# Optimization experiments

Hardware: AMD Instinct MI355X
Metric: run time of the kernel (lower is better)

## Reference

```python
import jax, jax.numpy as jnp
import numpy as np

N = 20000      # nodes
E = 640000     # edges (before self-loops)
F = 64         # base node feature len
H = 2          # heads per layer
EPS = 1e-5
NEG_SLOPE = 0.2  # PyG GATConv leaky_relu slope


def setup_inputs():
    key = jax.random.key(0)
    ks = jax.random.split(key, 16)
    s = 0.1
    x = jax.random.normal(ks[0], (N, F), jnp.float32)
    edge_index = jax.random.randint(ks[1], (2, E), 0, N, dtype=jnp.int64)
    # layer 1: in=F, heads=H, out-per-head C1=F -> out dim H*F=128
    C1 = F
    W1 = jax.random.normal(ks[2], (F, H * C1), jnp.float32) * s
    att_src1 = jax.random.normal(ks[3], (H, C1), jnp.float32) * s
    att_dst1 = jax.random.normal(ks[4], (H, C1), jnp.float32) * s
    bias1 = jnp.zeros((H * C1,), jnp.float32)
    gamma1 = jnp.ones((H * C1,), jnp.float32)
    beta1 = jnp.zeros((H * C1,), jnp.float32)
    # layer 2: in=H*F=128, heads=H, out-per-head C2=H*F -> out dim H*H*F=256
    C2 = H * F
    W2 = jax.random.normal(ks[5], (H * C1, H * C2), jnp.float32) * s
    att_src2 = jax.random.normal(ks[6], (H, C2), jnp.float32) * s
    att_dst2 = jax.random.normal(ks[7], (H, C2), jnp.float32) * s
    bias2 = jnp.zeros((H * C2,), jnp.float32)
    gamma2 = jnp.ones((H * C2,), jnp.float32)
    beta2 = jnp.zeros((H * C2,), jnp.float32)
    return {"x": x, "edge_index": edge_index,
            "W1": W1, "att_src1": att_src1, "att_dst1": att_dst1, "bias1": bias1,
            "gamma1": gamma1, "beta1": beta1,
            "W2": W2, "att_src2": att_src2, "att_dst2": att_dst2, "bias2": bias2,
            "gamma2": gamma2, "beta2": beta2}


def _gat_conv(x, src, dst, W, att_src, att_dst, bias):
    # PyG GATConv (concat=True, add_self_loops already applied to src/dst)
    n = x.shape[0]
    h, c = att_src.shape
    hx = (x @ W).reshape(n, h, c)                       # [N,H,C]
    a_s = jnp.einsum('nhc,hc->nh', hx, att_src)         # [N,H]
    a_d = jnp.einsum('nhc,hc->nh', hx, att_dst)
    e = a_s[src] + a_d[dst]                             # [E',H]
    e = jnp.where(e > 0, e, NEG_SLOPE * e)              # leaky relu
    # segment softmax over incoming edges of each target node
    m = jax.ops.segment_max(e, dst, num_segments=n)     # [N,H]
    p = jnp.exp(e - m[dst])
    z = jax.ops.segment_sum(p, dst, num_segments=n)     # [N,H]
    alpha = p / z[dst]                                  # [E',H]
    msg = hx[src] * alpha[:, :, None]                   # [E',H,C]
    out = jax.ops.segment_sum(msg, dst, num_segments=n) # [N,H,C]
    return out.reshape(n, h * c) + bias


def _batch_norm(x, gamma, beta):
    mu = x.mean(axis=0)
    var = x.var(axis=0)  # biased, matches torch BN normalization
    return (x - mu) * jax.lax.rsqrt(var + EPS) * gamma + beta


def reference(x, edge_index, W1, att_src1, att_dst1, bias1, gamma1, beta1,
              W2, att_src2, att_dst2, bias2, gamma2, beta2):
    loops = jnp.arange(N, dtype=edge_index.dtype)
    src = jnp.concatenate([edge_index[0], loops])
    dst = jnp.concatenate([edge_index[1], loops])
    h = _gat_conv(x, src, dst, W1, att_src1, att_dst1, bias1)
    h = jax.nn.relu(_batch_norm(h, gamma1, beta1))
    h = _gat_conv(h, src, dst, W2, att_src2, att_dst2, bias2)
    h = jax.nn.relu(_batch_norm(h, gamma2, beta2))
    return h
```

## Files before the change

### kernel.cpp

```cpp
#include <hip/hip_runtime.h>
#include <hip/hip_bf16.h>
#include <math.h>

#define NN 20000
#define ER 640000
#define ET 660000
#define HH 2
#define D1 128
#define D2 256
#define EPSV 1e-5f
#define SLOPE 0.2f

typedef __attribute__((ext_vector_type(8))) short bf16x8;
typedef __attribute__((ext_vector_type(4))) float f32x4;


__device__ __forceinline__ int detect64(const void* ei) {
  const int* p = (const int*)ei;
  return (p[1] | p[3] | p[5] | p[7]) == 0;
}
__device__ __forceinline__ int clampn(int v) { return v < 0 ? 0 : (v >= NN ? NN-1 : v); }
__device__ __forceinline__ float bf16_lo(unsigned int u){ return __uint_as_float(u<<16); }
__device__ __forceinline__ float bf16_hi(unsigned int u){ return __uint_as_float(u & 0xffff0000u); }

__global__ void k_front(const void* ei, const float* W1, const float* W2,
                        __hip_bfloat16* W1t, __hip_bfloat16* W2c, int* dpart, int* gcount) {
  extern __shared__ int hist[];
  int b = blockIdx.x, t = threadIdx.x;
  if (b == 0 && t == 0) *gcount = 0;
  if (b < 160) {
    int i = b*256 + t;
    if (i < 8192) {
      int n = i >> 6, k = i & 63;
      W1t[i] = __float2bfloat16(W1[k*128 + n]);
    } else {
      int i2 = i - 8192;
      int kc = i2 >> 13, n = (i2 >> 5) & 255, kk = i2 & 31;
      W2c[i2] = __float2bfloat16(W2[(kc*32 + kk)*256 + n]);
    }
    return;
  }
  int db = b - 160;
  for (int i = t; i < NN; i += 256) hist[i] = 0;
  __syncthreads();
  int is64 = detect64(ei);
  int base = db * 80000;
  if (is64) {
    const long long* p64 = (const long long*)ei;
    for (int i = base + t*4; i < base + 80000; i += 1024) {
      uint4 qa = *(const uint4*)(p64 + ER + i);
      uint4 qb = *(const uint4*)(p64 + ER + i + 2);
      atomicAdd(&hist[clampn((int)qa.x)], 1);
      atomicAdd(&hist[clampn((int)qa.z)], 1);
      atomicAdd(&hist[clampn((int)qb.x)], 1);
      atomicAdd(&hist[clampn((int)qb.z)], 1);
    }
  } else {
    const int* p32 = (const int*)ei;
    for (int i = base + t*4; i < base + 80000; i += 1024) {
      uint4 q = *(const uint4*)(p32 + ER + i);
      atomicAdd(&hist[clampn((int)q.x)], 1);
      atomicAdd(&hist[clampn((int)q.y)], 1);
      atomicAdd(&hist[clampn((int)q.z)], 1);
      atomicAdd(&hist[clampn((int)q.w)], 1);
    }
  }
  __syncthreads();
  for (int i = t; i < NN; i += 256) dpart[db*NN + i] = hist[i];
}

__global__ __launch_bounds__(256) void k_alloc(const int* dpart, int* begv, int* endv,
                                               int* cursor, int* gcount, float* bnz) {
  __shared__ int wsum[4], wbase[4];
  int gid = blockIdx.x*256 + threadIdx.x;
  if (gid < 768) bnz[gid] = 0.f;
  int d = 0;
  if (gid < NN) {
    d = 1;
    #pragma unroll
    for (int bb = 0; bb < 8; bb++) d += dpart[bb*NN + gid];
  }
  int lane = threadIdx.x & 63, w = threadIdx.x >> 6;
  int v = d;
  #pragma unroll
  for (int o = 1; o < 64; o <<= 1) {
    int u = __shfl_up(v, o);
    if (lane >= o) v += u;
  }
  if (lane == 63) wsum[w] = v;
  __syncthreads();
  if (threadIdx.x == 0) {
    int s0 = wsum[0], s1 = wsum[1], s2 = wsum[2], s3 = wsum[3];
    int b = atomicAdd(gcount, s0 + s1 + s2 + s3);
    wbase[0] = b; wbase[1] = b + s0; wbase[2] = b + s0 + s1; wbase[3] = b + s0 + s1 + s2;
  }
  __syncthreads();
  if (gid < NN) {
    int beg = wbase[w] + v - d;
    begv[gid] = beg; cursor[gid] = beg; endv[gid] = beg + d;
  }
}

__global__ void k_scatter(const void* ei, int* cursor, int* srcs) {
  int i0 = (blockIdx.x*256 + threadIdx.x)*4;
  if (i0 >= ET) return;
  int s[4], d[4];
  if (i0 >= ER) {
    #pragma unroll
    for (int k = 0; k < 4; k++) { s[k] = i0 + k - ER; d[k] = s[k]; }
  } else if (detect64(ei)) {
    const long long* p64 = (const long long*)ei;
    uint4 qa = *(const uint4*)(p64 + i0);
    uint4 qb = *(const uint4*)(p64 + i0 + 2);
    uint4 ra = *(const uint4*)(p64 + ER + i0);
    uint4 rb = *(const uint4*)(p64 + ER + i0 + 2);
    s[0]=clampn((int)qa.x); s[1]=clampn((int)qa.z); s[2]=clampn((int)qb.x); s[3]=clampn((int)qb.z);
    d[0]=clampn((int)ra.x); d[1]=clampn((int)ra.z); d[2]=clampn((int)rb.x); d[3]=clampn((int)rb.z);
  } else {
    const int* p32 = (const int*)ei;
    uint4 qs = *(const uint4*)(p32 + i0);
    uint4 qd = *(const uint4*)(p32 + ER + i0);
    s[0]=clampn((int)qs.x); s[1]=clampn((int)qs.y); s[2]=clampn((int)qs.z); s[3]=clampn((int)qs.w);
    d[0]=clampn((int)qd.x); d[1]=clampn((int)qd.y); d[2]=clampn((int)qd.z); d[3]=clampn((int)qd.w);
  }
  #pragma unroll
  for (int k = 0; k < 4; k++) {
    int pos = atomicAdd(&cursor[d[k]], 1);
    srcs[pos] = s[k];
  }
}

__global__ __launch_bounds__(256) void k_gemm1f(const float* x, const __hip_bfloat16* W1t,
                                                const float* att_s1, const float* att_d1,
                                                __hip_bfloat16* hxb, float2* as1, float2* ad1) {
  __shared__ __hip_bfloat16 As[64][72];
  __shared__ __hip_bfloat16 Bs[128][72];
  __shared__ float asred[4][64], adred[4][64];
  int t = threadIdx.x;
  int m0 = blockIdx.x * 64;
  for (int i = t; i < 512; i += 256) {
    int r = i >> 3, s = i & 7;
    int gr = m0 + r; if (gr >= NN) gr = NN - 1;
    float4 f0 = ((const float4*)(x + (size_t)gr*64))[s*2];
    float4 f1 = ((const float4*)(x + (size_t)gr*64))[s*2+1];
    __hip_bfloat16 hb[8] = {
      __float2bfloat16(f0.x), __float2bfloat16(f0.y), __float2bfloat16(f0.z), __float2bfloat16(f0.w),
      __float2bfloat16(f1.x), __float2bfloat16(f1.y), __float2bfloat16(f1.z), __float2bfloat16(f1.w)};
    *(uint4*)&As[r][s*8] = *(uint4*)hb;
  }
  for (int i = t; i < 1024; i += 256) {
    int r = i >> 3, s = i & 7;
    *(uint4*)&Bs[r][s*8] = ((const uint4*)(W1t + (size_t)r*64))[s];
  }
  __syncthreads();
  int w = t >> 6, lane = t & 63;
  int lm = lane & 15, q = lane >> 4;
  f32x4 acc[4][2];
  #pragma unroll
  for (int rt = 0; rt < 4; rt++)
    #pragma unroll
    for (int ct = 0; ct < 2; ct++) acc[rt][ct] = (f32x4){0.f,0.f,0.f,0.f};
  #pragma unroll
  for (int kc = 0; kc < 2; kc++) {
    bf16x8 bfr[2];
    #pragma unroll
    for (int ct = 0; ct < 2; ct++)
      bfr[ct] = *(const bf16x8*)&Bs[w*32 + ct*16 + lm][kc*32 + q*8];
    #pragma unroll
    for (int rt = 0; rt < 4; rt++) {
      bf16x8 a = *(const bf16x8*)&As[rt*16 + lm][kc*32 + q*8];
      acc[rt][0] = __builtin_amdgcn_mfma_f32_16x16x32_bf16(a, bfr[0], acc[rt][0], 0, 0, 0);
      acc[rt][1] = __builtin_amdgcn_mfma_f32_16x16x32_bf16(a, bfr[1], acc[rt][1], 0, 0, 0);
    }
  }
  #pragma unroll
  for (int rt = 0; rt < 4; rt++)
    #pragma unroll
    for (int ct = 0; ct < 2; ct++)
      #pragma unroll
      for (int rg = 0; rg < 4; rg++) {
        int row = m0 + rt*16 + q*4 + rg;
        int col = w*32 + ct*16 + lm;
        if (row < NN) hxb[(size_t)row*128 + col] = __float2bfloat16(acc[rt][ct][rg]);
      }
  float asc[2], adc[2];
  #pragma unroll
  for (int ct = 0; ct < 2; ct++) {
    int col = w*32 + ct*16 + lm;
    asc[ct] = att_s1[col]; adc[ct] = att_d1[col];
  }
  #pragma unroll
  for (int rt = 0; rt < 4; rt++)
    #pragma unroll
    for (int rg = 0; rg < 4; rg++) {
      float ps = acc[rt][0][rg]*asc[0] + acc[rt][1][rg]*asc[1];
      float pd = acc[rt][0][rg]*adc[0] + acc[rt][1][rg]*adc[1];
      #pragma unroll
      for (int o = 1; o < 16; o <<= 1) { ps += __shfl_xor(ps, o); pd += __shfl_xor(pd, o); }
      if (lm == 0) { int row = rt*16 + q*4 + rg; asred[w][row] = ps; adred[w][row] = pd; }
    }
  __syncthreads();
  if (t < 64) {
    int row = m0 + t;
    if (row < NN) {
      as1[row] = make_float2(asred[0][t] + asred[1][t], asred[2][t] + asred[3][t]);
      ad1[row] = make_float2(adred[0][t] + adred[1][t], adred[2][t] + adred[3][t]);
    }
  }
}

__global__ __launch_bounds__(256) void k_gemm2f(const float* out1, const __hip_bfloat16* W2c,
                                                const float* bns1, const float* bnq1,
                                                const float* gamma1, const float* beta1,
                                                const float* att_s2, const float* att_d2,
                                                __hip_bfloat16* hxb, float2* as2, float2* ad2) {
  __shared__ __hip_bfloat16 As[64][136];
  __shared__ __hip_bfloat16 Bs[256][40];
  __shared__ float AB[2][128];
  __shared__ float asred[4][64], adred[4][64];
  int t = threadIdx.x;
  int m0 = blockIdx.x * 64;
  if (t < 128) {
    float mean = bns1[t]*(1.f/NN);
    float var  = bnq1[t]*(1.f/NN) - mean*mean;
    float A = rsqrtf(var + EPSV)*gamma1[t];
    AB[0][t] = A; AB[1][t] = beta1[t] - mean*A;
  }
  __syncthreads();
  for (int i = t; i < 1024; i += 256) {
    int r = i >> 4, s = i & 15;
    int gr = m0 + r; if (gr >= NN) gr = NN - 1;
    float4 f0 = ((const float4*)(out1 + (size_t)gr*128))[s*2];
    float4 f1 = ((const float4*)(out1 + (size_t)gr*128))[s*2+1];
    int c = s*8;
    float v[8] = {f0.x,f0.y,f0.z,f0.w,f1.x,f1.y,f1.z,f1.w};
    __hip_bfloat16 hb[8];
    #pragma unroll
    for (int k = 0; k < 8; k++)
      hb[k] = __float2bfloat16(fmaxf(v[k]*AB[0][c+k] + AB[1][c+k], 0.f));
    *(uint4*)&As[r][s*8] = *(uint4*)hb;
  }
  int w = t >> 6, lane = t & 63;
  int lm = lane & 15, q = lane >> 4;
  f32x4 acc[4][4];
  #pragma unroll
  for (int rt = 0; rt < 4; rt++)
    #pragma unroll
    for (int ct = 0; ct < 4; ct++) acc[rt][ct] = (f32x4){0.f,0.f,0.f,0.f};
  for (int kc = 0; kc < 4; kc++) {
    __syncthreads();
    for (int i = t; i < 1024; i += 256) {
      int r = i >> 2, s = i & 3;
      *(uint4*)&Bs[r][s*8] = ((const uint4*)(W2c + ((size_t)kc*256 + r)*32))[s];
    }
    __syncthreads();
    bf16x8 bfr[4];
    #pragma unroll
    for (int ct = 0; ct < 4; ct++)
      bfr[ct] = *(const bf16x8*)&Bs[w*64 + ct*16 + lm][q*8];
    #pragma unroll
    for (int rt = 0; rt < 4; rt++) {
      bf16x8 a = *(const bf16x8*)&As[rt*16 + lm][kc*32 + q*8];
      #pragma unroll
      for (int ct = 0; ct < 4; ct++)
        acc[rt][ct] = __builtin_amdgcn_mfma_f32_16x16x32_bf16(a, bfr[ct], acc[rt][ct], 0, 0, 0);
    }
  }
  #pragma unroll
  for (int rt = 0; rt < 4; rt++)
    #pragma unroll
    for (int ct = 0; ct < 4; ct++)
      #pragma unroll
      for (int rg = 0; rg < 4; rg++) {
        int row = m0 + rt*16 + q*4 + rg;
        int col = w*64 + ct*16 + lm;
        if (row < NN) hxb[(size_t)row*256 + col] = __float2bfloat16(acc[rt][ct][rg]);
      }
  float asc[4], adc[4];
  #pragma unroll
  for (int ct = 0; ct < 4; ct++) {
    int col = w*64 + ct*16 + lm;
    asc[ct] = att_s2[col]; adc[ct] = att_d2[col];
  }
  #pragma unroll
  for (int rt = 0; rt < 4; rt++)
    #pragma unroll
    for (int rg = 0; rg < 4; rg++) {
      float ps = acc[rt][0][rg]*asc[0] + acc[rt][1][rg]*asc[1]
               + acc[rt][2][rg]*asc[2] + acc[rt][3][rg]*asc[3];
      float pd = acc[rt][0][rg]*adc[0] + acc[rt][1][rg]*adc[1]
               + acc[rt][2][rg]*adc[2] + acc[rt][3][rg]*adc[3];
      #pragma unroll
      for (int o = 1; o < 16; o <<= 1) { ps += __shfl_xor(ps, o); pd += __shfl_xor(pd, o); }
      if (lm == 0) { int row = rt*16 + q*4 + rg; asred[w][row] = ps; adred[w][row] = pd; }
    }
  __syncthreads();
  if (t < 64) {
    int row = m0 + t;
    if (row < NN) {
      as2[row] = make_float2(asred[0][t] + asred[1][t], asred[2][t] + asred[3][t]);
      ad2[row] = make_float2(adred[0][t] + adred[1][t], adred[2][t] + adred[3][t]);
    }
  }
}

__global__ __launch_bounds__(64) void k_agg1(const int* begv, const int* endv, const int* srcs,
                                             const float2* asv, const float2* adv,
                                             const uint2* hx, const float* bias, float* out) {
  __shared__ float2 sp[2][64];
  int n = blockIdx.x, t = threadIdx.x;
  int l = t & 31, eo = t >> 5;
  int h = l >> 4;
  float2 ad = adv[n];
  int beg = begv[n], end = endv[n];
  float a0=0.f,a1=0.f,a2=0.f,a3=0.f,z0=0.f,z1=0.f;
  for (int cb = beg; cb < end; cb += 64) {
    int len = end - cb; if (len > 64) len = 64;
    if (t < len) {
      int s = srcs[cb + t];
      float2 as = asv[s];
      float e0 = as.x + ad.x, e1 = as.y + ad.y;
      e0 = e0 > 0.f ? e0 : SLOPE*e0;
      e1 = e1 > 0.f ? e1 : SLOPE*e1;
      float p0 = __expf(e0), p1 = __expf(e1);
      sp[0][t] = make_float2(__int_as_float(s), p0);
      sp[1][t] = make_float2(__int_as_float(s), p1);
      z0 += p0; z1 += p1;
    }
    __syncthreads();
    for (int j = eo; j < len; j += 2) {
      float2 v = sp[h][j];
      uint2 u = hx[(size_t)__float_as_int(v.x)*32 + l];
      a0 += v.y*bf16_lo(u.x); a1 += v.y*bf16_hi(u.x);
      a2 += v.y*bf16_lo(u.y); a3 += v.y*bf16_hi(u.y);
    }
    __syncthreads();
  }
  a0 += __shfl_down(a0, 32); a1 += __shfl_down(a1, 32);
  a2 += __shfl_down(a2, 32); a3 += __shfl_down(a3, 32);
  #pragma unroll
  for (int o = 1; o < 64; o <<= 1) { z0 += __shfl_xor(z0, o); z1 += __shfl_xor(z1, o); }
  if (t < 32) {
    float inv = 1.f / (h ? z1 : z0);
    float4 b4 = ((const float4*)bias)[t];
    float4 o4 = { a0*inv + b4.x, a1*inv + b4.y, a2*inv + b4.z, a3*inv + b4.w };
    ((float4*)(out + (size_t)n*D1))[t] = o4;
  }
}

__global__ __launch_bounds__(64) void k_agg2(const int* begv, const int* endv, const int* srcs,
                                             const float2* asv, const float2* adv,
                                             const uint2* hx, const float* bias, float* out) {
  __shared__ float2 sp[2][64];
  int n = blockIdx.x, t = threadIdx.x;
  int h = t >> 5;
  float2 ad = adv[n];
  int beg = begv[n], end = endv[n];
  float a0=0.f,a1=0.f,a2=0.f,a3=0.f,z0=0.f,z1=0.f;
  for (int cb = beg; cb < end; cb += 64) {
    int len = end - cb; if (len > 64) len = 64;
    if (t < len) {
      int s = srcs[cb + t];
      float2 as = asv[s];
      float e0 = as.x + ad.x, e1 = as.y + ad.y;
      e0 = e0 > 0.f ? e0 : SLOPE*e0;
      e1 = e1 > 0.f ? e1 : SLOPE*e1;
      float p0 = __expf(e0), p1 = __expf(e1);
      sp[0][t] = make_float2(__int_as_float(s), p0);
      sp[1][t] = make_float2(__int_as_float(s), p1);
      z0 += p0; z1 += p1;
    }
    __syncthreads();
    int j = 0;
    for (; j + 1 < len; j += 2) {
      float2 v0 = sp[h][j], v1 = sp[h][j+1];
      uint2 u0 = hx[(size_t)__float_as_int(v0.x)*64 + t];
      uint2 u1 = hx[(size_t)__float_as_int(v1.x)*64 + t];
      a0 += v0.y*bf16_lo(u0.x) + v1.y*bf16_lo(u1.x);
      a1 += v0.y*bf16_hi(u0.x) + v1.y*bf16_hi(u1.x);
      a2 += v0.y*bf16_lo(u0.y) + v1.y*bf16_lo(u1.y);
      a3 += v0.y*bf16_hi(u0.y) + v1.y*bf16_hi(u1.y);
    }
    for (; j < len; j++) {
      float2 v = sp[h][j];
      uint2 u = hx[(size_t)__float_as_int(v.x)*64 + t];
      a0 += v.y*bf16_lo(u.x); a1 += v.y*bf16_hi(u.x);
      a2 += v.y*bf16_lo(u.y); a3 += v.y*bf16_hi(u.y);
    }
    __syncthreads();
  }
  #pragma unroll
  for (int o = 1; o < 64; o <<= 1) { z0 += __shfl_xor(z0, o); z1 += __shfl_xor(z1, o); }
  float inv = 1.f / (h ? z1 : z0);
  float4 b4 = ((const float4*)bias)[t];
  float4 o4 = { a0*inv + b4.x, a1*inv + b4.y, a2*inv + b4.z, a3*inv + b4.w };
  ((float4*)(out + (size_t)n*D2))[t] = o4;
}

template<int D>
__global__ void k_bnstats(const float* x, float* bnsum, float* bnsq) {
  const int ROWS = 100;
  int c = threadIdx.x;
  int r0 = blockIdx.x * ROWS;
  float s = 0.f, s2 = 0.f;
  for (int r = 0; r < ROWS; r++) {
    float v = x[(size_t)(r0 + r)*D + c];
    s += v; s2 += v*v;
  }
  atomicAdd(&bnsum[c], s);
  atomicAdd(&bnsq[c], s2);
}

__global__ void k_bnapply2(const float* x, const float* bnsum, const float* bnsq,
                           const float* gamma, const float* beta, float* out) {
  int i = blockIdx.x*blockDim.x + threadIdx.x;
  if (i >= NN*D2/4) return;
  int c = (i & 63) * 4;
  float4 v = ((const float4*)x)[i];
  float r[4] = {v.x, v.y, v.z, v.w};
  #pragma unroll
  for (int k = 0; k < 4; k++) {
    float mean = bnsum[c+k] * (1.f/NN);
    float var  = bnsq[c+k] * (1.f/NN) - mean*mean;
    float o = (r[k] - mean) * rsqrtf(var + EPSV) * gamma[c+k] + beta[c+k];
    r[k] = o > 0.f ? o : 0.f;
  }
  float4 o4 = {r[0], r[1], r[2], r[3]};
  ((float4*)out)[i] = o4;
}

extern "C" void kernel_launch(void* const* d_in, const int* in_sizes, int n_in,
                              void* d_out, int out_size, void* d_ws, size_t ws_size,
                              hipStream_t stream) {
  const float* x      = (const float*)d_in[0];
  const void*  ei     = d_in[1];
  const float* W1     = (const float*)d_in[2];
  const float* att_s1 = (const float*)d_in[3];
  const float* att_d1 = (const float*)d_in[4];
  const float* bias1  = (const float*)d_in[5];
  const float* gamma1 = (const float*)d_in[6];
  const float* beta1  = (const float*)d_in[7];
  const float* W2     = (const float*)d_in[8];
  const float* att_s2 = (const float*)d_in[9];
  const float* att_d2 = (const float*)d_in[10];
  const float* bias2  = (const float*)d_in[11];
  const float* gamma2 = (const float*)d_in[12];
  const float* beta2  = (const float*)d_in[13];

  char* p = (char*)d_ws;
  __hip_bfloat16* hx1b = (__hip_bfloat16*)p; p += (size_t)NN*D1*2;
  __hip_bfloat16* hx2b = (__hip_bfloat16*)p; p += (size_t)NN*D2*2;
  __hip_bfloat16* W1t  = (__hip_bfloat16*)p; p += 8192*2;
  __hip_bfloat16* W2c  = (__hip_bfloat16*)p; p += 32768*2;
  float* out1 = (float*)p; p += (size_t)NN*D1*4;
  float* out2 = (float*)p; p += (size_t)NN*D2*4;
  float2* as1 = (float2*)p; p += (size_t)NN*8;
  float2* ad1 = (float2*)p; p += (size_t)NN*8;
  float2* as2 = (float2*)p; p += (size_t)NN*8;
  float2* ad2 = (float2*)p; p += (size_t)NN*8;
  float* bns1 = (float*)p; p += D1*4;
  float* bnq1 = (float*)p; p += D1*4;
  float* bns2 = (float*)p; p += D2*4;
  float* bnq2 = (float*)p; p += D2*4;
  int* dpart  = (int*)p; p += (size_t)8*NN*4;
  int* begv   = (int*)p; p += NN*4;
  int* endv   = (int*)p; p += NN*4;
  int* cursor = (int*)p; p += NN*4;
  int* gcount = (int*)p; p += 16*4;
  int* srcs   = (int*)p; p += (size_t)ET*4;

  k_front<<<168, 256, NN*sizeof(int), stream>>>(ei, W1, W2, W1t, W2c, dpart, gcount);
  k_alloc<<<(NN+255)/256, 256, 0, stream>>>(dpart, begv, endv, cursor, gcount, bns1);
  k_scatter<<<(ET/4 + 255)/256, 256, 0, stream>>>(ei, cursor, srcs);

  k_gemm1f<<<(NN+63)/64, 256, 0, stream>>>(x, W1t, att_s1, att_d1, hx1b, as1, ad1);
  k_agg1<<<NN, 64, 0, stream>>>(begv, endv, srcs, as1, ad1, (const uint2*)hx1b, bias1, out1);
  k_bnstats<D1><<<200, D1, 0, stream>>>(out1, bns1, bnq1);

  k_gemm2f<<<(NN+63)/64, 256, 0, stream>>>(out1, W2c, bns1, bnq1, gamma1, beta1,
                                           att_s2, att_d2, hx2b, as2, ad2);
  k_agg2<<<NN, 64, 0, stream>>>(begv, endv, srcs, as2, ad2, (const uint2*)hx2b, bias2, out2);
  k_bnstats<D2><<<200, D2, 0, stream>>>(out2, bns2, bnq2);
  k_bnapply2<<<(NN*D2/4 + 255)/256, 256, 0, stream>>>(out2, bns2, bnq2, gamma2, beta2,
                                                      (float*)d_out);
}
```

Baseline: 274.6 us.

## Fuse whole GAT pipeline into one persistent cooperative kernel with grid syncs

Replaces the chain of about ten separate kernel launches with a single persistent cooperative kernel that walks seven phases, separated by grid-wide syncs. The edge histogram now uses packed 16-bit counters in 64 chunks. BatchNorm statistics are accumulated inside the aggregation phases instead of in separate stats kernels. Weight bf16 conversion is folded into each GEMM tile, and aggregation now processes one node per wave across a grid-stride loop. This removes launch gaps and extra passes over the output, at the cost of lower occupancy, grid-sync overhead, and redundant weight conversion in every tile.

```diff
diff --git a/kernel.cpp b/kernel.cpp
--- a/kernel.cpp
+++ b/kernel.cpp
@@ -1,19 +1,40 @@
 #include <hip/hip_runtime.h>
 #include <hip/hip_bf16.h>
+#include <hip/hip_cooperative_groups.h>
 #include <math.h>
 
 #define NN 20000
 #define ER 640000
 #define ET 660000
-#define HH 2
 #define D1 128
 #define D2 256
 #define EPSV 1e-5f
 #define SLOPE 0.2f
+#define NT1 313
+#define NHIST 64
+#define HCH 10000
 
 typedef __attribute__((ext_vector_type(8))) short bf16x8;
 typedef __attribute__((ext_vector_type(4))) float f32x4;
 
+namespace cg = cooperative_groups;
+
+struct P {
+  const float* x; const void* ei;
+  const float* W1; const float* att_s1; const float* att_d1; const float* bias1;
+  const float* gamma1; const float* beta1;
+  const float* W2; const float* att_s2; const float* att_d2; const float* bias2;
+  const float* gamma2; const float* beta2;
+  __hip_bfloat16* hx1b; __hip_bfloat16* hx2b;
+  float* out1; float* out2;
+  float2* as1; float2* ad1; float2* as2; float2* ad2;
+  float* bn;
+  unsigned int* dpart;
+  int* begv; int* endv; int* cursor; int* gcount;
+  int* srcs;
+  float* dout;
+  int ph_lo, ph_hi, coop;
+};
 
 __device__ __forceinline__ int detect64(const void* ei) {
   const int* p = (const int*)ei;
@@ -23,138 +44,29 @@
 __device__ __forceinline__ float bf16_lo(unsigned int u){ return __uint_as_float(u<<16); }
 __device__ __forceinline__ float bf16_hi(unsigned int u){ return __uint_as_float(u & 0xffff0000u); }
 
-__global__ void k_front(const void* ei, const float* W1, const float* W2,
-                        __hip_bfloat16* W1t, __hip_bfloat16* W2c, int* dpart, int* gcount) {
-  extern __shared__ int hist[];
-  int b = blockIdx.x, t = threadIdx.x;
-  if (b == 0 && t == 0) *gcount = 0;
-  if (b < 160) {
-    int i = b*256 + t;
-    if (i < 8192) {
-      int n = i >> 6, k = i & 63;
-      W1t[i] = __float2bfloat16(W1[k*128 + n]);
-    } else {
-      int i2 = i - 8192;
-      int kc = i2 >> 13, n = (i2 >> 5) & 255, kk = i2 & 31;
-      W2c[i2] = __float2bfloat16(W2[(kc*32 + kk)*256 + n]);
-    }
-    return;
-  }
-  int db = b - 160;
-  for (int i = t; i < NN; i += 256) hist[i] = 0;
-  __syncthreads();
-  int is64 = detect64(ei);
-  int base = db * 80000;
-  if (is64) {
-    const long long* p64 = (const long long*)ei;
-    for (int i = base + t*4; i < base + 80000; i += 1024) {
-      uint4 qa = *(const uint4*)(p64 + ER + i);
-      uint4 qb = *(const uint4*)(p64 + ER + i + 2);
-      atomicAdd(&hist[clampn((int)qa.x)], 1);
-      atomicAdd(&hist[clampn((int)qa.z)], 1);
-      atomicAdd(&hist[clampn((int)qb.x)], 1);
-      atomicAdd(&hist[clampn((int)qb.z)], 1);
-    }
-  } else {
-    const int* p32 = (const int*)ei;
-    for (int i = base + t*4; i < base + 80000; i += 1024) {
-      uint4 q = *(const uint4*)(p32 + ER + i);
-      atomicAdd(&hist[clampn((int)q.x)], 1);
-      atomicAdd(&hist[clampn((int)q.y)], 1);
-      atomicAdd(&hist[clampn((int)q.z)], 1);
-      atomicAdd(&hist[clampn((int)q.w)], 1);
-    }
-  }
-  __syncthreads();
-  for (int i = t; i < NN; i += 256) dpart[db*NN + i] = hist[i];
-}
-
-__global__ __launch_bounds__(256) void k_alloc(const int* dpart, int* begv, int* endv,
-                                               int* cursor, int* gcount, float* bnz) {
-  __shared__ int wsum[4], wbase[4];
-  int gid = blockIdx.x*256 + threadIdx.x;
-  if (gid < 768) bnz[gid] = 0.f;
-  int d = 0;
-  if (gid < NN) {
-    d = 1;
-    #pragma unroll
-    for (int bb = 0; bb < 8; bb++) d += dpart[bb*NN + gid];
-  }
-  int lane = threadIdx.x & 63, w = threadIdx.x >> 6;
-  int v = d;
-  #pragma unroll
-  for (int o = 1; o < 64; o <<= 1) {
-    int u = __shfl_up(v, o);
-    if (lane >= o) v += u;
-  }
-  if (lane == 63) wsum[w] = v;
-  __syncthreads();
-  if (threadIdx.x == 0) {
-    int s0 = wsum[0], s1 = wsum[1], s2 = wsum[2], s3 = wsum[3];
-    int b = atomicAdd(gcount, s0 + s1 + s2 + s3);
-    wbase[0] = b; wbase[1] = b + s0; wbase[2] = b + s0 + s1; wbase[3] = b + s0 + s1 + s2;
-  }
-  __syncthreads();
-  if (gid < NN) {
-    int beg = wbase[w] + v - d;
-    begv[gid] = beg; cursor[gid] = beg; endv[gid] = beg + d;
-  }
-}
-
-__global__ void k_scatter(const void* ei, int* cursor, int* srcs) {
-  int i0 = (blockIdx.x*256 + threadIdx.x)*4;
-  if (i0 >= ET) return;
-  int s[4], d[4];
-  if (i0 >= ER) {
-    #pragma unroll
-    for (int k = 0; k < 4; k++) { s[k] = i0 + k - ER; d[k] = s[k]; }
-  } else if (detect64(ei)) {
-    const long long* p64 = (const long long*)ei;
-    uint4 qa = *(const uint4*)(p64 + i0);
-    uint4 qb = *(const uint4*)(p64 + i0 + 2);
-    uint4 ra = *(const uint4*)(p64 + ER + i0);
-    uint4 rb = *(const uint4*)(p64 + ER + i0 + 2);
-    s[0]=clampn((int)qa.x); s[1]=clampn((int)qa.z); s[2]=clampn((int)qb.x); s[3]=clampn((int)qb.z);
-    d[0]=clampn((int)ra.x); d[1]=clampn((int)ra.z); d[2]=clampn((int)rb.x); d[3]=clampn((int)rb.z);
-  } else {
-    const int* p32 = (const int*)ei;
-    uint4 qs = *(const uint4*)(p32 + i0);
-    uint4 qd = *(const uint4*)(p32 + ER + i0);
-    s[0]=clampn((int)qs.x); s[1]=clampn((int)qs.y); s[2]=clampn((int)qs.z); s[3]=clampn((int)qs.w);
-    d[0]=clampn((int)qd.x); d[1]=clampn((int)qd.y); d[2]=clampn((int)qd.z); d[3]=clampn((int)qd.w);
-  }
-  #pragma unroll
-  for (int k = 0; k < 4; k++) {
-    int pos = atomicAdd(&cursor[d[k]], 1);
-    srcs[pos] = s[k];
-  }
-}
-
-__global__ __launch_bounds__(256) void k_gemm1f(const float* x, const __hip_bfloat16* W1t,
-                                                const float* att_s1, const float* att_d1,
-                                                __hip_bfloat16* hxb, float2* as1, float2* ad1) {
-  __shared__ __hip_bfloat16 As[64][72];
-  __shared__ __hip_bfloat16 Bs[128][72];
-  __shared__ float asred[4][64], adred[4][64];
+__device__ void gemm1_tile(int u, const P& p, char* smem) {
+  auto As = (__hip_bfloat16 (*)[72])smem;
+  auto Bs = (__hip_bfloat16 (*)[72])(smem + 9216);
+  float* asred = (float*)(smem + 27648);
+  float* adred = (float*)(smem + 28672);
   int t = threadIdx.x;
-  int m0 = blockIdx.x * 64;
+  int m0 = u * 64;
   for (int i = t; i < 512; i += 256) {
     int r = i >> 3, s = i & 7;
     int gr = m0 + r; if (gr >= NN) gr = NN - 1;
-    float4 f0 = ((const float4*)(x + (size_t)gr*64))[s*2];
-    float4 f1 = ((const float4*)(x + (size_t)gr*64))[s*2+1];
+    float4 f0 = ((const float4*)(p.x + (size_t)gr*64))[s*2];
+    float4 f1 = ((const float4*)(p.x + (size_t)gr*64))[s*2+1];
     __hip_bfloat16 hb[8] = {
       __float2bfloat16(f0.x), __float2bfloat16(f0.y), __float2bfloat16(f0.z), __float2bfloat16(f0.w),
       __float2bfloat16(f1.x), __float2bfloat16(f1.y), __float2bfloat16(f1.z), __float2bfloat16(f1.w)};
     *(uint4*)&As[r][s*8] = *(uint4*)hb;
   }
-  for (int i = t; i < 1024; i += 256) {
-    int r = i >> 3, s = i & 7;
-    *(uint4*)&Bs[r][s*8] = ((const uint4*)(W1t + (size_t)r*64))[s];
-  }
-  __syncthreads();
-  int w = t >> 6, lane = t & 63;
-  int lm = lane & 15, q = lane >> 4;
+  for (int i = t; i < 8192; i += 256) {
+    int n = i & 127, k = i >> 7;
+    Bs[n][k] = __float2bfloat16(p.W1[k*128 + n]);
+  }
+  __syncthreads();
+  int w = t >> 6, lane = t & 63, lm = lane & 15, q = lane >> 4;
   f32x4 acc[4][2];
   #pragma unroll
   for (int rt = 0; rt < 4; rt++)
@@ -181,13 +93,13 @@
       for (int rg = 0; rg < 4; rg++) {
         int row = m0 + rt*16 + q*4 + rg;
         int col = w*32 + ct*16 + lm;
-        if (row < NN) hxb[(size_t)row*128 + col] = __float2bfloat16(acc[rt][ct][rg]);
+        if (row < NN) p.hx1b[(size_t)row*128 + col] = __float2bfloat16(acc[rt][ct][rg]);
       }
   float asc[2], adc[2];
   #pragma unroll
   for (int ct = 0; ct < 2; ct++) {
     int col = w*32 + ct*16 + lm;
-    asc[ct] = att_s1[col]; adc[ct] = att_d1[col];
+    asc[ct] = p.att_s1[col]; adc[ct] = p.att_d1[col];
   }
   #pragma unroll
   for (int rt = 0; rt < 4; rt++)
@@ -197,51 +109,182 @@
       float pd = acc[rt][0][rg]*adc[0] + acc[rt][1][rg]*adc[1];
       #pragma unroll
       for (int o = 1; o < 16; o <<= 1) { ps += __shfl_xor(ps, o); pd += __shfl_xor(pd, o); }
-      if (lm == 0) { int row = rt*16 + q*4 + rg; asred[w][row] = ps; adred[w][row] = pd; }
+      if (lm == 0) { int row = rt*16 + q*4 + rg; asred[w*64+row] = ps; adred[w*64+row] = pd; }
     }
   __syncthreads();
   if (t < 64) {
     int row = m0 + t;
     if (row < NN) {
-      as1[row] = make_float2(asred[0][t] + asred[1][t], asred[2][t] + asred[3][t]);
-      ad1[row] = make_float2(adred[0][t] + adred[1][t], adred[2][t] + adred[3][t]);
-    }
-  }
-}
-
-__global__ __launch_bounds__(256) void k_gemm2f(const float* out1, const __hip_bfloat16* W2c,
-                                                const float* bns1, const float* bnq1,
-                                                const float* gamma1, const float* beta1,
-                                                const float* att_s2, const float* att_d2,
-                                                __hip_bfloat16* hxb, float2* as2, float2* ad2) {
-  __shared__ __hip_bfloat16 As[64][136];
-  __shared__ __hip_bfloat16 Bs[256][40];
-  __shared__ float AB[2][128];
-  __shared__ float asred[4][64], adred[4][64];
+      p.as1[row] = make_float2(asred[t] + asred[64+t], asred[128+t] + asred[192+t]);
+      p.ad1[row] = make_float2(adred[t] + adred[64+t], adred[128+t] + adred[192+t]);
+    }
+  }
+  __syncthreads();
+}
+
+__device__ void hist_unit(int db, const P& p, char* smem) {
+  unsigned int* hist = (unsigned int*)smem;
   int t = threadIdx.x;
-  int m0 = blockIdx.x * 64;
+  for (int i = t; i < HCH; i += 256) hist[i] = 0;
+  __syncthreads();
+  int base = db * HCH;
+  if (detect64(p.ei)) {
+    const long long* q = (const long long*)p.ei + ER;
+    for (int i = base + t; i < base + HCH; i += 256) {
+      int d = clampn((int)q[i]);
+      atomicAdd(&hist[d>>1], 1u << ((d&1)*16));
+    }
+  } else {
+    const int* q = (const int*)p.ei + ER;
+    for (int i = base + t; i < base + HCH; i += 256) {
+      int d = clampn(q[i]);
+      atomicAdd(&hist[d>>1], 1u << ((d&1)*16));
+    }
+  }
+  __syncthreads();
+  for (int i = t; i < HCH; i += 256) p.dpart[db*HCH + i] = hist[i];
+  __syncthreads();
+}
+
+__device__ void alloc_unit(int u, const P& p, char* smem) {
+  int* wsum  = (int*)smem;
+  int* wbase = wsum + 4;
+  int t = threadIdx.x;
+  int gid = u*256 + t;
+  int d = 0;
+  if (gid < NN) {
+    d = 1;
+    int half = (gid & 1) * 16;
+    int idx = gid >> 1;
+    for (int db = 0; db < NHIST; db++)
+      d += (p.dpart[db*HCH + idx] >> half) & 0xffff;
+  }
+  int lane = t & 63, w = t >> 6;
+  int v = d;
+  #pragma unroll
+  for (int o = 1; o < 64; o <<= 1) {
+    int uu = __shfl_up(v, o);
+    if (lane >= o) v += uu;
+  }
+  if (lane == 63) wsum[w] = v;
+  __syncthreads();
+  if (t == 0) {
+    int s0 = wsum[0], s1 = wsum[1], s2 = wsum[2], s3 = wsum[3];
+    int b = atomicAdd(p.gcount, s0 + s1 + s2 + s3);
+    wbase[0] = b; wbase[1] = b + s0; wbase[2] = b + s0 + s1; wbase[3] = b + s0 + s1 + s2;
+  }
+  __syncthreads();
+  if (gid < NN) {
+    int beg = wbase[w] + v - d;
+    p.begv[gid] = beg; p.cursor[gid] = beg; p.endv[gid] = beg + d;
+  }
+  __syncthreads();
+}
+
+__device__ void scatter_phase(const P& p, int gtid, int GT) {
+  int is64 = detect64(p.ei);
+  for (int u = gtid; u < ET/4; u += GT) {
+    int i0 = u*4;
+    int s[4], d[4];
+    if (i0 >= ER) {
+      #pragma unroll
+      for (int k = 0; k < 4; k++) { s[k] = i0 + k - ER; d[k] = s[k]; }
+    } else if (is64) {
+      const long long* p64 = (const long long*)p.ei;
+      uint4 qa = *(const uint4*)(p64 + i0);
+      uint4 qb = *(const uint4*)(p64 + i0 + 2);
+      uint4 ra = *(const uint4*)(p64 + ER + i0);
+      uint4 rb = *(const uint4*)(p64 + ER + i0 + 2);
+      s[0]=clampn((int)qa.x); s[1]=clampn((int)qa.z); s[2]=clampn((int)qb.x); s[3]=clampn((int)qb.z);
+      d[0]=clampn((int)ra.x); d[1]=clampn((int)ra.z); d[2]=clampn((int)rb.x); d[3]=clampn((int)rb.z);
+    } else {
+      const int* p32 = (const int*)p.ei;
+      uint4 qs = *(const uint4*)(p32 + i0);
+      uint4 qd = *(const uint4*)(p32 + ER + i0);
+      s[0]=clampn((int)qs.x); s[1]=clampn((int)qs.y); s[2]=clampn((int)qs.z); s[3]=clampn((int)qs.w);
+      d[0]=clampn((int)qd.x); d[1]=clampn((int)qd.y); d[2]=clampn((int)qd.z); d[3]=clampn((int)qd.w);
+    }
+    #pragma unroll
+    for (int k = 0; k < 4; k++) {
+      int pos = atomicAdd(&p.cursor[d[k]], 1);
+      p.srcs[pos] = s[k];
+    }
+  }
+}
+
+__device__ void agg1_phase(const P& p, char* smem, int B) {
+  float* bnacc = (float*)smem;
+  int t = threadIdx.x;
+  for (int i = t; i < 256; i += 256) bnacc[i] = 0.f;
+  __syncthreads();
+  int wid = t >> 6, lane = t & 63, h = lane >> 5;
+  const unsigned int* hx = (const unsigned int*)p.hx1b;
+  for (int n = blockIdx.x*4 + wid; n < NN; n += B*4) {
+    float2 ad = p.ad1[n];
+    int beg = p.begv[n], end = p.endv[n];
+    float a0=0.f, a1=0.f, z0=0.f, z1=0.f;
+    for (int cb = beg; cb < end; cb += 64) {
+      int len = end - cb; if (len > 64) len = 64;
+      int st = 0; float p0 = 0.f, p1 = 0.f;
+      if (lane < len) {
+        st = p.srcs[cb + lane];
+        float2 as = p.as1[st];
+        float e0 = as.x + ad.x, e1 = as.y + ad.y;
+        e0 = e0 > 0.f ? e0 : SLOPE*e0;
+        e1 = e1 > 0.f ? e1 : SLOPE*e1;
+        p0 = __expf(e0); p1 = __expf(e1);
+        z0 += p0; z1 += p1;
+      }
+      for (int j = 0; j < len; j++) {
+        int sj = __shfl(st, j);
+        float q0 = __shfl(p0, j), q1 = __shfl(p1, j);
+        float pj = h ? q1 : q0;
+        unsigned int uu = hx[(size_t)sj*64 + lane];
+        a0 += pj*bf16_lo(uu); a1 += pj*bf16_hi(uu);
+      }
+    }
+    #pragma unroll
+    for (int o = 1; o < 64; o <<= 1) { z0 += __shfl_xor(z0, o); z1 += __shfl_xor(z1, o); }
+    float inv = 1.f / (h ? z1 : z0);
+    float v0 = a0*inv + p.bias1[2*lane];
+    float v1 = a1*inv + p.bias1[2*lane+1];
+    ((float2*)(p.out1 + (size_t)n*D1))[lane] = make_float2(v0, v1);
+    atomicAdd(&bnacc[2*lane], v0);       atomicAdd(&bnacc[2*lane+1], v1);
+    atomicAdd(&bnacc[128+2*lane], v0*v0); atomicAdd(&bnacc[128+2*lane+1], v1*v1);
+  }
+  __syncthreads();
+  for (int i = t; i < 256; i += 256) atomicAdd(&p.bn[i], bnacc[i]);
+}
+
+__device__ void gemm2_tile(int u, const P& p, char* smem) {
+  auto As = (__hip_bfloat16 (*)[136])smem;
+  auto Bs = (__hip_bfloat16 (*)[40])(smem + 17408);
+  float* AB    = (float*)(smem + 37888);
+  float* asred = (float*)(smem + 38912);
+  float* adred = (float*)(smem + 39936);
+  int t = threadIdx.x;
+  int m0 = u * 64;
   if (t < 128) {
-    float mean = bns1[t]*(1.f/NN);
-    float var  = bnq1[t]*(1.f/NN) - mean*mean;
-    float A = rsqrtf(var + EPSV)*gamma1[t];
-    AB[0][t] = A; AB[1][t] = beta1[t] - mean*A;
+    float mean = p.bn[t]*(1.f/NN);
+    float var  = p.bn[128+t]*(1.f/NN) - mean*mean;
+    float A = rsqrtf(var + EPSV)*p.gamma1[t];
+    AB[t] = A; AB[128+t] = p.beta1[t] - mean*A;
   }
   __syncthreads();
   for (int i = t; i < 1024; i += 256) {
     int r = i >> 4, s = i & 15;
     int gr = m0 + r; if (gr >= NN) gr = NN - 1;
-    float4 f0 = ((const float4*)(out1 + (size_t)gr*128))[s*2];
-    float4 f1 = ((const float4*)(out1 + (size_t)gr*128))[s*2+1];
+    float4 f0 = ((const float4*)(p.out1 + (size_t)gr*128))[s*2];
+    float4 f1 = ((const float4*)(p.out1 + (size_t)gr*128))[s*2+1];
     int c = s*8;
     float v[8] = {f0.x,f0.y,f0.z,f0.w,f1.x,f1.y,f1.z,f1.w};
     __hip_bfloat16 hb[8];
     #pragma unroll
     for (int k = 0; k < 8; k++)
-      hb[k] = __float2bfloat16(fmaxf(v[k]*AB[0][c+k] + AB[1][c+k], 0.f));
+      hb[k] = __float2bfloat16(fmaxf(v[k]*AB[c+k] + AB[128+c+k], 0.f));
     *(uint4*)&As[r][s*8] = *(uint4*)hb;
   }
-  int w = t >> 6, lane = t & 63;
-  int lm = lane & 15, q = lane >> 4;
+  int w = t >> 6, lane = t & 63, lm = lane & 15, q = lane >> 4;
   f32x4 acc[4][4];
   #pragma unroll
   for (int rt = 0; rt < 4; rt++)
@@ -249,9 +292,9 @@
     for (int ct = 0; ct < 4; ct++) acc[rt][ct] = (f32x4){0.f,0.f,0.f,0.f};
   for (int kc = 0; kc < 4; kc++) {
     __syncthreads();
-    for (int i = t; i < 1024; i += 256) {
-      int r = i >> 2, s = i & 3;
-      *(uint4*)&Bs[r][s*8] = ((const uint4*)(W2c + ((size_t)kc*256 + r)*32))[s];
+    for (int i = t; i < 8192; i += 256) {
+      int n = i & 255, kk = i >> 8;
+      Bs[n][kk] = __float2bfloat16(p.W2[(kc*32 + kk)*256 + n]);
     }
     __syncthreads();
     bf16x8 bfr[4];
@@ -274,13 +317,13 @@
       for (int rg = 0; rg < 4; rg++) {
         int row = m0 + rt*16 + q*4 + rg;
         int col = w*64 + ct*16 + lm;
-        if (row < NN) hxb[(size_t)row*256 + col] = __float2bfloat16(acc[rt][ct][rg]);
+        if (row < NN) p.hx2b[(size_t)row*256 + col] = __float2bfloat16(acc[rt][ct][rg]);
       }
   float asc[4], adc[4];
   #pragma unroll
   for (int ct = 0; ct < 4; ct++) {
     int col = w*64 + ct*16 + lm;
-    asc[ct] = att_s2[col]; adc[ct] = att_d2[col];
+    asc[ct] = p.att_s2[col]; adc[ct] = p.att_d2[col];
   }
   #pragma unroll
   for (int rt = 0; rt < 4; rt++)
@@ -292,195 +335,171 @@
                + acc[rt][2][rg]*adc[2] + acc[rt][3][rg]*adc[3];
       #pragma unroll
       for (int o = 1; o < 16; o <<= 1) { ps += __shfl_xor(ps, o); pd += __shfl_xor(pd, o); }
-      if (lm == 0) { int row = rt*16 + q*4 + rg; asred[w][row] = ps; adred[w][row] = pd; }
+      if (lm == 0) { int row = rt*16 + q*4 + rg; asred[w*64+row] = ps; adred[w*64+row] = pd; }
     }
   __syncthreads();
   if (t < 64) {
     int row = m0 + t;
     if (row < NN) {
-      as2[row] = make_float2(asred[0][t] + asred[1][t], asred[2][t] + asred[3][t]);
-      ad2[row] = make_float2(adred[0][t] + adred[1][t], adred[2][t] + adred[3][t]);
-    }
-  }
-}
-
-__global__ __launch_bounds__(64) void k_agg1(const int* begv, const int* endv, const int* srcs,
-                                             const float2* asv, const float2* adv,
-                                             const uint2* hx, const float* bias, float* out) {
-  __shared__ float2 sp[2][64];
-  int n = blockIdx.x, t = threadIdx.x;
-  int l = t & 31, eo = t >> 5;
-  int h = l >> 4;
-  float2 ad = adv[n];
-  int beg = begv[n], end = endv[n];
-  float a0=0.f,a1=0.f,a2=0.f,a3=0.f,z0=0.f,z1=0.f;
-  for (int cb = beg; cb < end; cb += 64) {
-    int len = end - cb; if (len > 64) len = 64;
-    if (t < len) {
-      int s = srcs[cb + t];
-      float2 as = asv[s];
-      float e0 = as.x + ad.x, e1 = as.y + ad.y;
-      e0 = e0 > 0.f ? e0 : SLOPE*e0;
-      e1 = e1 > 0.f ? e1 : SLOPE*e1;
-      float p0 = __expf(e0), p1 = __expf(e1);
-      sp[0][t] = make_float2(__int_as_float(s), p0);
-      sp[1][t] = make_float2(__int_as_float(s), p1);
-      z0 += p0; z1 += p1;
-    }
-    __syncthreads();
-    for (int j = eo; j < len; j += 2) {
-      float2 v = sp[h][j];
-      uint2 u = hx[(size_t)__float_as_int(v.x)*32 + l];
-      a0 += v.y*bf16_lo(u.x); a1 += v.y*bf16_hi(u.x);
-      a2 += v.y*bf16_lo(u.y); a3 += v.y*bf16_hi(u.y);
-    }
-    __syncthreads();
-  }
-  a0 += __shfl_down(a0, 32); a1 += __shfl_down(a1, 32);
-  a2 += __shfl_down(a2, 32); a3 += __shfl_down(a3, 32);
-  #pragma unroll
-  for (int o = 1; o < 64; o <<= 1) { z0 += __shfl_xor(z0, o); z1 += __shfl_xor(z1, o); }
-  if (t < 32) {
+      p.as2[row] = make_float2(asred[t] + asred[64+t], asred[128+t] + asred[192+t]);
+      p.ad2[row] = make_float2(adred[t] + adred[64+t], adred[128+t] + adred[192+t]);
+    }
+  }
+  __syncthreads();
+}
+
+__device__ void agg2_phase(const P& p, char* smem, int B) {
+  float* bnacc = (float*)smem;
+  int t = threadIdx.x;
+  for (int i = t; i < 512; i += 256) bnacc[i] = 0.f;
+  __syncthreads();
+  int wid = t >> 6, lane = t & 63, h = lane >> 5;
+  const uint2* hx = (const uint2*)p.hx2b;
+  for (int n = blockIdx.x*4 + wid; n < NN; n += B*4) {
+    float2 ad = p.ad2[n];
+    int beg = p.begv[n], end = p.endv[n];
+    float a0=0.f,a1=0.f,a2=0.f,a3=0.f,z0=0.f,z1=0.f;
+    for (int cb = beg; cb < end; cb += 64) {
+      int len = end - cb; if (len > 64) len = 64;
+      int st = 0; float p0 = 0.f, p1 = 0.f;
+      if (lane < len) {
+        st = p.srcs[cb + lane];
+        float2 as = p.as2[st];
+        float e0 = as.x + ad.x, e1 = as.y + ad.y;
+        e0 = e0 > 0.f ? e0 : SLOPE*e0;
+        e1 = e1 > 0.f ? e1 : SLOPE*e1;
+        p0 = __expf(e0); p1 = __expf(e1);
+        z0 += p0; z1 += p1;
+      }
+      for (int j = 0; j < len; j++) {
+        int sj = __shfl(st, j);
+        float q0 = __shfl(p0, j), q1 = __shfl(p1, j);
+        float pj = h ? q1 : q0;
+        uint2 uu = hx[(size_t)sj*64 + lane];
+        a0 += pj*bf16_lo(uu.x); a1 += pj*bf16_hi(uu.x);
+        a2 += pj*bf16_lo(uu.y); a3 += pj*bf16_hi(uu.y);
+      }
+    }
+    #pragma unroll
+    for (int o = 1; o < 64; o <<= 1) { z0 += __shfl_xor(z0, o); z1 += __shfl_xor(z1, o); }
     float inv = 1.f / (h ? z1 : z0);
-    float4 b4 = ((const float4*)bias)[t];
+    float4 b4 = ((const float4*)p.bias2)[lane];
     float4 o4 = { a0*inv + b4.x, a1*inv + b4.y, a2*inv + b4.z, a3*inv + b4.w };
-    ((float4*)(out + (size_t)n*D1))[t] = o4;
-  }
-}
-
-__global__ __launch_bounds__(64) void k_agg2(const int* begv, const int* endv, const int* srcs,
-                                             const float2* asv, const float2* adv,
-                                             const uint2* hx, const float* bias, float* out) {
-  __shared__ float2 sp[2][64];
-  int n = blockIdx.x, t = threadIdx.x;
-  int h = t >> 5;
-  float2 ad = adv[n];
-  int beg = begv[n], end = endv[n];
-  float a0=0.f,a1=0.f,a2=0.f,a3=0.f,z0=0.f,z1=0.f;
-  for (int cb = beg; cb < end; cb += 64) {
-    int len = end - cb; if (len > 64) len = 64;
-    if (t < len) {
-      int s = srcs[cb + t];
-      float2 as = asv[s];
-      float e0 = as.x + ad.x, e1 = as.y + ad.y;
-      e0 = e0 > 0.f ? e0 : SLOPE*e0;
-      e1 = e1 > 0.f ? e1 : SLOPE*e1;
-      float p0 = __expf(e0), p1 = __expf(e1);
-      sp[0][t] = make_float2(__int_as_float(s), p0);
-      sp[1][t] = make_float2(__int_as_float(s), p1);
-      z0 += p0; z1 += p1;
-    }
-    __syncthreads();
-    int j = 0;
-    for (; j + 1 < len; j += 2) {
-      float2 v0 = sp[h][j], v1 = sp[h][j+1];
-      uint2 u0 = hx[(size_t)__float_as_int(v0.x)*64 + t];
-      uint2 u1 = hx[(size_t)__float_as_int(v1.x)*64 + t];
-      a0 += v0.y*bf16_lo(u0.x) + v1.y*bf16_lo(u1.x);
-      a1 += v0.y*bf16_hi(u0.x) + v1.y*bf16_hi(u1.x);
-      a2 += v0.y*bf16_lo(u0.y) + v1.y*bf16_lo(u1.y);
-      a3 += v0.y*bf16_hi(u0.y) + v1.y*bf16_hi(u1.y);
-    }
-    for (; j < len; j++) {
-      float2 v = sp[h][j];
-      uint2 u = hx[(size_t)__float_as_int(v.x)*64 + t];
-      a0 += v.y*bf16_lo(u.x); a1 += v.y*bf16_hi(u.x);
-      a2 += v.y*bf16_lo(u.y); a3 += v.y*bf16_hi(u.y);
-    }
-    __syncthreads();
-  }
-  #pragma unroll
-  for (int o = 1; o < 64; o <<= 1) { z0 += __shfl_xor(z0, o); z1 += __shfl_xor(z1, o); }
-  float inv = 1.f / (h ? z1 : z0);
-  float4 b4 = ((const float4*)bias)[t];
-  float4 o4 = { a0*inv + b4.x, a1*inv + b4.y, a2*inv + b4.z, a3*inv + b4.w };
-  ((float4*)(out + (size_t)n*D2))[t] = o4;
-}
-
-template<int D>
-__global__ void k_bnstats(const float* x, float* bnsum, float* bnsq) {
-  const int ROWS = 100;
-  int c = threadIdx.x;
-  int r0 = blockIdx.x * ROWS;
-  float s = 0.f, s2 = 0.f;
-  for (int r = 0; r < ROWS; r++) {
-    float v = x[(size_t)(r0 + r)*D + c];
-    s += v; s2 += v*v;
-  }
-  atomicAdd(&bnsum[c], s);
-  atomicAdd(&bnsq[c], s2);
-}
-
-__global__ void k_bnapply2(const float* x, const float* bnsum, const float* bnsq,
-                           const float* gamma, const float* beta, float* out) {
-  int i = blockIdx.x*blockDim.x + threadIdx.x;
-  if (i >= NN*D2/4) return;
-  int c = (i & 63) * 4;
-  float4 v = ((const float4*)x)[i];
-  float r[4] = {v.x, v.y, v.z, v.w};
-  #pragma unroll
-  for (int k = 0; k < 4; k++) {
-    float mean = bnsum[c+k] * (1.f/NN);
-    float var  = bnsq[c+k] * (1.f/NN) - mean*mean;
-    float o = (r[k] - mean) * rsqrtf(var + EPSV) * gamma[c+k] + beta[c+k];
-    r[k] = o > 0.f ? o : 0.f;
-  }
-  float4 o4 = {r[0], r[1], r[2], r[3]};
-  ((float4*)out)[i] = o4;
+    ((float4*)(p.out2 + (size_t)n*D2))[lane] = o4;
+    int c = 4*lane;
+    atomicAdd(&bnacc[c],   o4.x); atomicAdd(&bnacc[c+1], o4.y);
+    atomicAdd(&bnacc[c+2], o4.z); atomicAdd(&bnacc[c+3], o4.w);
+    atomicAdd(&bnacc[256+c],   o4.x*o4.x); atomicAdd(&bnacc[256+c+1], o4.y*o4.y);
+    atomicAdd(&bnacc[256+c+2], o4.z*o4.z); atomicAdd(&bnacc[256+c+3], o4.w*o4.w);
+  }
+  __syncthreads();
+  for (int i = t; i < 512; i += 256) atomicAdd(&p.bn[256+i], bnacc[i]);
+}
+
+__global__ __launch_bounds__(256, 4) void k_mono(P p) {
+  __shared__ __attribute__((aligned(16))) char smem[40960];
+  cg::grid_group g = cg::this_grid();
+  int B = gridDim.x, bid = blockIdx.x, t = threadIdx.x;
+  int gtid = bid*256 + t, GT = B*256;
+  for (int ph = p.ph_lo; ph < p.ph_hi; ph++) {
+    switch (ph) {
+      case 0:
+        for (int u = bid; u < NT1 + NHIST + 1; u += B) {
+          if (u < NT1) gemm1_tile(u, p, smem);
+          else if (u < NT1 + NHIST) hist_unit(u - NT1, p, smem);
+          else {
+            if (t == 0) *p.gcount = 0;
+            for (int i = t; i < 768; i += 256) p.bn[i] = 0.f;
+          }
+        }
+        break;
+      case 1:
+        for (int u = bid; u < (NN + 255)/256; u += B) alloc_unit(u, p, smem);
+        break;
+      case 2: scatter_phase(p, gtid, GT); break;
+      case 3: agg1_phase(p, smem, B); break;
+      case 4:
+        for (int u = bid; u < NT1; u += B) gemm2_tile(u, p, smem);
+        break;
+      case 5: agg2_phase(p, smem, B); break;
+      case 6:
+        for (int i = gtid; i < NN*64; i += GT) {
+          int c = (i & 63)*4;
+          float4 v = ((const float4*)p.out2)[i];
+          float r[4] = {v.x, v.y, v.z, v.w};
+          #pragma unroll
+          for (int k = 0; k < 4; k++) {
+            float mean = p.bn[256+c+k]*(1.f/NN);
+            float var  = p.bn[512+c+k]*(1.f/NN) - mean*mean;
+            float o = (r[k] - mean)*rsqrtf(var + EPSV)*p.gamma2[c+k] + p.beta2[c+k];
+            r[k] = o > 0.f ? o : 0.f;
+          }
+          float4 o4 = {r[0], r[1], r[2], r[3]};
+          ((float4*)p.dout)[i] = o4;
+        }
+        break;
+    }
+    if (p.coop && ph + 1 < p.ph_hi) g.sync();
+  }
 }
 
 extern "C" void kernel_launch(void* const* d_in, const int* in_sizes, int n_in,
                               void* d_out, int out_size, void* d_ws, size_t ws_size,
                               hipStream_t stream) {
-  const float* x      = (const float*)d_in[0];
-  const void*  ei     = d_in[1];
-  const float* W1     = (const float*)d_in[2];
-  const float* att_s1 = (const float*)d_in[3];
-  const float* att_d1 = (const float*)d_in[4];
-  const float* bias1  = (const float*)d_in[5];
-  const float* gamma1 = (const float*)d_in[6];
-  const float* beta1  = (const float*)d_in[7];
-  const float* W2     = (const float*)d_in[8];
-  const float* att_s2 = (const float*)d_in[9];
-  const float* att_d2 = (const float*)d_in[10];
-  const float* bias2  = (const float*)d_in[11];
-  const float* gamma2 = (const float*)d_in[12];
-  const float* beta2  = (const float*)d_in[13];
+  P prm;
+  prm.x      = (const float*)d_in[0];
+  prm.ei     = d_in[1];
+  prm.W1     = (const float*)d_in[2];
+  prm.att_s1 = (const float*)d_in[3];
+  prm.att_d1 = (const float*)d_in[4];
+  prm.bias1  = (const float*)d_in[5];
+  prm.gamma1 = (const float*)d_in[6];
+  prm.beta1  = (const float*)d_in[7];
+  prm.W2     = (const float*)d_in[8];
+  prm.att_s2 = (const float*)d_in[9];
+  prm.att_d2 = (const float*)d_in[10];
+  prm.bias2  = (const float*)d_in[11];
+  prm.gamma2 = (const float*)d_in[12];
+  prm.beta2  = (const float*)d_in[13];
 
   char* p = (char*)d_ws;
-  __hip_bfloat16* hx1b = (__hip_bfloat16*)p; p += (size_t)NN*D1*2;
-  __hip_bfloat16* hx2b = (__hip_bfloat16*)p; p += (size_t)NN*D2*2;
-  __hip_bfloat16* W1t  = (__hip_bfloat16*)p; p += 8192*2;
-  __hip_bfloat16* W2c  = (__hip_bfloat16*)p; p += 32768*2;
-  float* out1 = (float*)p; p += (size_t)NN*D1*4;
-  float* out2 = (float*)p; p += (size_t)NN*D2*4;
-  float2* as1 = (float2*)p; p += (size_t)NN*8;
-  float2* ad1 = (float2*)p; p += (size_t)NN*8;
-  float2* as2 = (float2*)p; p += (size_t)NN*8;
-  float2* ad2 = (float2*)p; p += (size_t)NN*8;
-  float* bns1 = (float*)p; p += D1*4;
-  float* bnq1 = (float*)p; p += D1*4;
-  float* bns2 = (float*)p; p += D2*4;
-  float* bnq2 = (float*)p; p += D2*4;
-  int* dpart  = (int*)p; p += (size_t)8*NN*4;
-  int* begv   = (int*)p; p += NN*4;
-  int* endv   = (int*)p; p += NN*4;
-  int* cursor = (int*)p; p += NN*4;
-  int* gcount = (int*)p; p += 16*4;
-  int* srcs   = (int*)p; p += (size_t)ET*4;
-
-  k_front<<<168, 256, NN*sizeof(int), stream>>>(ei, W1, W2, W1t, W2c, dpart, gcount);
-  k_alloc<<<(NN+255)/256, 256, 0, stream>>>(dpart, begv, endv, cursor, gcount, bns1);
-  k_scatter<<<(ET/4 + 255)/256, 256, 0, stream>>>(ei, cursor, srcs);
-
-  k_gemm1f<<<(NN+63)/64, 256, 0, stream>>>(x, W1t, att_s1, att_d1, hx1b, as1, ad1);
-  k_agg1<<<NN, 64, 0, stream>>>(begv, endv, srcs, as1, ad1, (const uint2*)hx1b, bias1, out1);
-  k_bnstats<D1><<<200, D1, 0, stream>>>(out1, bns1, bnq1);
-
-  k_gemm2f<<<(NN+63)/64, 256, 0, stream>>>(out1, W2c, bns1, bnq1, gamma1, beta1,
-                                           att_s2, att_d2, hx2b, as2, ad2);
-  k_agg2<<<NN, 64, 0, stream>>>(begv, endv, srcs, as2, ad2, (const uint2*)hx2b, bias2, out2);
-  k_bnstats<D2><<<200, D2, 0, stream>>>(out2, bns2, bnq2);
-  k_bnapply2<<<(NN*D2/4 + 255)/256, 256, 0, stream>>>(out2, bns2, bnq2, gamma2, beta2,
-                                                      (float*)d_out);
-}
+  prm.hx1b = (__hip_bfloat16*)p; p += (size_t)NN*D1*2;
+  prm.hx2b = (__hip_bfloat16*)p; p += (size_t)NN*D2*2;
+  prm.out1 = (float*)p; p += (size_t)NN*D1*4;
+  prm.out2 = (float*)p; p += (size_t)NN*D2*4;
+  prm.as1  = (float2*)p; p += (size_t)NN*8;
+  prm.ad1  = (float2*)p; p += (size_t)NN*8;
+  prm.as2  = (float2*)p; p += (size_t)NN*8;
+  prm.ad2  = (float2*)p; p += (size_t)NN*8;
+  prm.bn   = (float*)p; p += 768*4;
+  prm.dpart = (unsigned int*)p; p += (size_t)NHIST*HCH*4;
+  prm.begv   = (int*)p; p += NN*4;
+  prm.endv   = (int*)p; p += NN*4;
+  prm.cursor = (int*)p; p += NN*4;
+  prm.gcount = (int*)p; p += 16*4;
+  prm.srcs   = (int*)p; p += (size_t)ET*4;
+  prm.dout = (float*)d_out;
+
+  int dev = 0; hipGetDevice(&dev);
+  int ncu = 0;
+  hipDeviceGetAttribute(&ncu, hipDeviceAttributeMultiprocessorCount, dev);
+  if (ncu <= 0) ncu = 256;
+  int coopSup = 0;
+  hipDeviceGetAttribute(&coopSup, hipDeviceAttributeCooperativeLaunch, dev);
+  int nb = 0;
+  if (hipOccupancyMaxActiveBlocksPerMultiprocessor(&nb, k_mono, 256, 0) != hipSuccess || nb < 1)
+    nb = 1;
+  if (nb > 4) nb = 4;
+  int grid = nb * ncu;
+
+  if (coopSup) {
+    prm.ph_lo = 0; prm.ph_hi = 7; prm.coop = 1;
+    void* args[] = { (void*)&prm };
+    hipLaunchCooperativeKernel(k_mono, dim3(grid), dim3(256), args, 0, stream);
+  } else {
+    for (int ph = 0; ph < 7; ph++) {
+      prm.ph_lo = ph; prm.ph_hi = ph + 1; prm.coop = 0;
+      k_mono<<<grid, 256, 0, stream>>>(prm);
+    }
+  }
+}
```

Result: slower. 866.2 us (+215.5%).
